# Performance work log

Measured on AMD Instinct MI355X. Metric: run time of the kernel, lower is better.

The kernel has to match this reference:

```python
import jax, jax.numpy as jnp
import numpy as np
from jax import lax

WINDOW_SIZE = 11
GAUSSIAN_SIGMA = 1.5
CROP_BORDER = 4
C1 = (0.01 * 255.0) ** 2
C2 = (0.03 * 255.0) ** 2


def _gaussian_kernel_window(ws: int, sigma: float) -> jnp.ndarray:
    # matches cv2.getGaussianKernel(ws, sigma) outer product
    x = jnp.arange(ws, dtype=jnp.float32) - (ws - 1) / 2.0
    g = jnp.exp(-(x ** 2) / (2.0 * sigma ** 2))
    g = g / jnp.sum(g)
    return jnp.outer(g, g)  # [ws, ws]


def _depthwise_conv(x: jnp.ndarray, kern: jnp.ndarray) -> jnp.ndarray:
    # x: [N, C, H, W]; kern: [C, 1, ws, ws]; valid padding, stride 1, groups=C
    return lax.conv_general_dilated(
        x, kern, window_strides=(1, 1), padding='VALID',
        dimension_numbers=('NCHW', 'OIHW', 'NCHW'),
        feature_group_count=x.shape[1])


def setup_inputs() -> dict:
    key = jax.random.key(0)
    k1, k2 = jax.random.split(key)
    raw_tensor = jax.random.uniform(k1, (32, 3, 512, 512), dtype=jnp.float32)
    dst_tensor = jax.random.uniform(k2, (32, 3, 512, 512), dtype=jnp.float32)
    return {"raw_tensor": raw_tensor, "dst_tensor": dst_tensor}


def reference(raw_tensor, dst_tensor):
    cb = CROP_BORDER
    raw = raw_tensor[:, :, cb:-cb, cb:-cb] * 255.0
    dst = dst_tensor[:, :, cb:-cb, cb:-cb] * 255.0
    C = raw.shape[1]
    kern = jnp.broadcast_to(
        _gaussian_kernel_window(WINDOW_SIZE, GAUSSIAN_SIGMA)[None, None],
        (C, 1, WINDOW_SIZE, WINDOW_SIZE)).astype(raw.dtype)

    raw_mean = _depthwise_conv(raw, kern)
    dst_mean = _depthwise_conv(dst, kern)
    raw_mean_sq = raw_mean ** 2
    dst_mean_sq = dst_mean ** 2
    raw_dst_mean = raw_mean * dst_mean
    raw_var = _depthwise_conv(raw * raw, kern) - raw_mean_sq
    dst_var = _depthwise_conv(dst * dst, kern) - dst_mean_sq
    raw_dst_cov = _depthwise_conv(raw * dst, kern) - raw_dst_mean

    num = (2.0 * raw_dst_mean + C1) * (2.0 * raw_dst_cov + C2)
    den = (raw_mean_sq + dst_mean_sq + C1) * (raw_var + dst_var + C2)
    ssim_map = num / den
    return jnp.mean(ssim_map, axis=(1, 2, 3)).astype(jnp.float32)  # [B]
```

## Files before the change

kernel.cpp:

```cpp
#include <hip/hip_runtime.h>


#define IMG   512
#define OUTD  494
#define CB    4
#define TW    64
#define TH    32
#define VSW   80
#define C1F   6.5025f
#define C2F   58.5225f
#define NPIX  732108.0f
#define XBLK  8
#define YBLK  16
#define SLOTS 384

__global__ __launch_bounds__(256) void ssim_main(
        const float* __restrict__ raw, const float* __restrict__ dst,
        float* __restrict__ partial) {
    __shared__ float vs[5][TH][VSW];
    __shared__ float red[4];

    const int tid = threadIdx.x;
    const int bc  = blockIdx.z;
    const int b   = bc / 3;
    const int c3  = bc - b * 3;
    const int ty0 = blockIdx.y * TH;
    const int tx0 = blockIdx.x * TW;

    float gw[11];
    {
        float s = 0.f;
        #pragma unroll
        for (int k = 0; k < 11; ++k) {
            float x = (float)(k - 5);
            gw[k] = expf(-x * x * (1.0f / 4.5f));
            s += gw[k];
        }
        float inv = 1.0f / s;
        #pragma unroll
        for (int k = 0; k < 11; ++k) gw[k] *= inv;
    }

    const float* rb = raw + (size_t)bc * (IMG * IMG);
    const float* db = dst + (size_t)bc * (IMG * IMG);

    #pragma unroll 1
    for (int t = tid; t < 304; t += 256) {
        const int rp = t / 19;
        const int xg = t - rp * 19;
        int col0 = CB + tx0 + xg * 4;
        if (col0 > IMG - 4) col0 = IMG - 4;
        const int row0 = CB + ty0 + rp * 2;

        float a0[5][4] = {{0.f}};
        float a1[5][4] = {{0.f}};
        #pragma unroll
        for (int k = 0; k < 12; ++k) {
            int r = row0 + k;
            if (r > IMG - 1) r = IMG - 1;
            const float4 va = *(const float4*)(rb + (size_t)r * IMG + col0);
            const float4 vc = *(const float4*)(db + (size_t)r * IMG + col0);
            const float A[4]  = {va.x, va.y, va.z, va.w};
            const float Cv[4] = {vc.x, vc.y, vc.z, vc.w};
            float p2[4], q2[4], pq[4];
            #pragma unroll
            for (int c = 0; c < 4; ++c) {
                p2[c] = A[c] * A[c];
                q2[c] = Cv[c] * Cv[c];
                pq[c] = A[c] * Cv[c];
            }
            if (k < 11) {
                const float w = gw[k];
                #pragma unroll
                for (int c = 0; c < 4; ++c) {
                    a0[0][c] = fmaf(w, A[c],  a0[0][c]);
                    a0[1][c] = fmaf(w, Cv[c], a0[1][c]);
                    a0[2][c] = fmaf(w, p2[c], a0[2][c]);
                    a0[3][c] = fmaf(w, q2[c], a0[3][c]);
                    a0[4][c] = fmaf(w, pq[c], a0[4][c]);
                }
            }
            if (k >= 1) {
                const float w = gw[k - 1];
                #pragma unroll
                for (int c = 0; c < 4; ++c) {
                    a1[0][c] = fmaf(w, A[c],  a1[0][c]);
                    a1[1][c] = fmaf(w, Cv[c], a1[1][c]);
                    a1[2][c] = fmaf(w, p2[c], a1[2][c]);
                    a1[3][c] = fmaf(w, q2[c], a1[3][c]);
                    a1[4][c] = fmaf(w, pq[c], a1[4][c]);
                }
            }
        }
        #pragma unroll
        for (int f = 0; f < 5; ++f) {
            *(float4*)&vs[f][rp * 2 + 0][xg * 4] =
                make_float4(a0[f][0], a0[f][1], a0[f][2], a0[f][3]);
            *(float4*)&vs[f][rp * 2 + 1][xg * 4] =
                make_float4(a1[f][0], a1[f][1], a1[f][2], a1[f][3]);
        }
    }
    __syncthreads();

    const int xg  = tid & 15;
    const int yt  = tid >> 4;
    const int ox0 = tx0 + xg * 4;
    float ssum = 0.f;
    #pragma unroll
    for (int r2 = 0; r2 < 2; ++r2) {
        const int row = yt * 2 + r2;
        const int oy  = ty0 + row;
        float m[5][4];
        #pragma unroll
        for (int f = 0; f < 5; ++f) {
            const float4* vp = (const float4*)&vs[f][row][xg * 4];
            const float4 A = vp[0], B = vp[1], Cq = vp[2], D = vp[3];
            const float win[16] = {A.x, A.y, A.z, A.w, B.x, B.y, B.z, B.w,
                                   Cq.x, Cq.y, Cq.z, Cq.w, D.x, D.y, D.z, D.w};
            #pragma unroll
            for (int c = 0; c < 4; ++c) {
                float o = 0.f;
                #pragma unroll
                for (int k = 0; k < 11; ++k) o = fmaf(gw[k], win[c + k], o);
                m[f][c] = o;
            }
        }
        if (oy < OUTD) {
            #pragma unroll
            for (int c = 0; c < 4; ++c) {
                if (ox0 + c < OUTD) {
                    const float mr  = m[0][c] * 255.0f;
                    const float md  = m[1][c] * 255.0f;
                    const float mrr = m[2][c] * 65025.0f;
                    const float mdd = m[3][c] * 65025.0f;
                    const float mrd = m[4][c] * 65025.0f;
                    const float mr2 = mr * mr, md2 = md * md, mpr = mr * md;
                    const float num = (2.0f * mpr + C1F) * (2.0f * (mrd - mpr) + C2F);
                    const float den = (mr2 + md2 + C1F) * ((mrr - mr2) + (mdd - md2) + C2F);
                    ssum += num / den;
                }
            }
        }
    }

    #pragma unroll
    for (int off = 32; off > 0; off >>= 1)
        ssum += __shfl_down(ssum, off, 64);
    const int lane = tid & 63, wv = tid >> 6;
    if (lane == 0) red[wv] = ssum;
    __syncthreads();
    if (tid == 0) {
        const float t = red[0] + red[1] + red[2] + red[3];
        partial[(size_t)b * SLOTS + (blockIdx.y * gridDim.x + blockIdx.x) * 3 + c3] = t;
    }
}

__global__ __launch_bounds__(128) void ssim_final(
        const float* __restrict__ partial, float* __restrict__ out) {
    __shared__ float red[2];
    const int b = blockIdx.x, tid = threadIdx.x;
    float s = 0.f;
    for (int i = tid; i < SLOTS; i += 128) s += partial[(size_t)b * SLOTS + i];
    #pragma unroll
    for (int off = 32; off > 0; off >>= 1) s += __shfl_down(s, off, 64);
    if ((tid & 63) == 0) red[tid >> 6] = s;
    __syncthreads();
    if (tid == 0) out[b] = (red[0] + red[1]) * (1.0f / NPIX);
}

extern "C" void kernel_launch(void* const* d_in, const int* in_sizes, int n_in,
                              void* d_out, int out_size, void* d_ws, size_t ws_size,
                              hipStream_t stream) {
    const float* raw = (const float*)d_in[0];
    const float* dst = (const float*)d_in[1];
    float* out     = (float*)d_out;
    float* partial = (float*)d_ws;

    dim3 grid(XBLK, YBLK, 96);
    ssim_main<<<grid, 256, 0, stream>>>(raw, dst, partial);
    ssim_final<<<32, 128, 0, stream>>>(partial, out);
}
```

Measured before the change: 275.1 us.

## Fold SSIM second-moment fields into sum-of-squares and squared-sum, widen horizontal pass

Replaces the three second-moment fields (r², d², rd) with two, r²+d² and (r+d)², so the covariance is recovered as ((r+d)² − (r²+d²))/2. This cuts the vertical-pass accumulators, the shared-memory intermediate and the horizontal convolutions from five fields to four. The horizontal pass now gives each thread one row of 8 outputs instead of two rows of 4, so neighbouring outputs share more of each loaded window. The launch bounds also request 4 blocks per SM, and the shared row stride shrinks. Recovering covariance by subtraction may cost some precision through cancellation.

```diff
diff --git a/kernel.cpp b/kernel.cpp
--- a/kernel.cpp
+++ b/kernel.cpp
@@ -6,7 +6,7 @@
 #define CB    4
 #define TW    64
 #define TH    32
-#define VSW   80
+#define VSW   76
 #define C1F   6.5025f
 #define C2F   58.5225f
 #define NPIX  732108.0f
@@ -14,10 +14,10 @@
 #define YBLK  16
 #define SLOTS 384
 
-__global__ __launch_bounds__(256) void ssim_main(
+__global__ __launch_bounds__(256, 4) void ssim_main(
         const float* __restrict__ raw, const float* __restrict__ dst,
         float* __restrict__ partial) {
-    __shared__ float vs[5][TH][VSW];
+    __shared__ float vs[4][TH][VSW];
     __shared__ float red[4];
 
     const int tid = threadIdx.x;
@@ -52,48 +52,46 @@
         if (col0 > IMG - 4) col0 = IMG - 4;
         const int row0 = CB + ty0 + rp * 2;
 
-        float a0[5][4] = {{0.f}};
-        float a1[5][4] = {{0.f}};
+        float a0[4][4] = {{0.f}};
+        float a1[4][4] = {{0.f}};
         #pragma unroll
         for (int k = 0; k < 12; ++k) {
             int r = row0 + k;
             if (r > IMG - 1) r = IMG - 1;
             const float4 va = *(const float4*)(rb + (size_t)r * IMG + col0);
             const float4 vc = *(const float4*)(db + (size_t)r * IMG + col0);
-            const float A[4]  = {va.x, va.y, va.z, va.w};
-            const float Cv[4] = {vc.x, vc.y, vc.z, vc.w};
-            float p2[4], q2[4], pq[4];
+            const float R[4] = {va.x, va.y, va.z, va.w};
+            const float D[4] = {vc.x, vc.y, vc.z, vc.w};
+            float s2[4], p2[4];
             #pragma unroll
             for (int c = 0; c < 4; ++c) {
-                p2[c] = A[c] * A[c];
-                q2[c] = Cv[c] * Cv[c];
-                pq[c] = A[c] * Cv[c];
+                const float u = R[c] + D[c];
+                s2[c] = fmaf(R[c], R[c], D[c] * D[c]);
+                p2[c] = u * u;
             }
             if (k < 11) {
                 const float w = gw[k];
                 #pragma unroll
                 for (int c = 0; c < 4; ++c) {
-                    a0[0][c] = fmaf(w, A[c],  a0[0][c]);
-                    a0[1][c] = fmaf(w, Cv[c], a0[1][c]);
-                    a0[2][c] = fmaf(w, p2[c], a0[2][c]);
-                    a0[3][c] = fmaf(w, q2[c], a0[3][c]);
-                    a0[4][c] = fmaf(w, pq[c], a0[4][c]);
+                    a0[0][c] = fmaf(w, R[c],  a0[0][c]);
+                    a0[1][c] = fmaf(w, D[c],  a0[1][c]);
+                    a0[2][c] = fmaf(w, s2[c], a0[2][c]);
+                    a0[3][c] = fmaf(w, p2[c], a0[3][c]);
                 }
             }
             if (k >= 1) {
                 const float w = gw[k - 1];
                 #pragma unroll
                 for (int c = 0; c < 4; ++c) {
-                    a1[0][c] = fmaf(w, A[c],  a1[0][c]);
-                    a1[1][c] = fmaf(w, Cv[c], a1[1][c]);
-                    a1[2][c] = fmaf(w, p2[c], a1[2][c]);
-                    a1[3][c] = fmaf(w, q2[c], a1[3][c]);
-                    a1[4][c] = fmaf(w, pq[c], a1[4][c]);
+                    a1[0][c] = fmaf(w, R[c],  a1[0][c]);
+                    a1[1][c] = fmaf(w, D[c],  a1[1][c]);
+                    a1[2][c] = fmaf(w, s2[c], a1[2][c]);
+                    a1[3][c] = fmaf(w, p2[c], a1[3][c]);
                 }
             }
         }
         #pragma unroll
-        for (int f = 0; f < 5; ++f) {
+        for (int f = 0; f < 4; ++f) {
             *(float4*)&vs[f][rp * 2 + 0][xg * 4] =
                 make_float4(a0[f][0], a0[f][1], a0[f][2], a0[f][3]);
             *(float4*)&vs[f][rp * 2 + 1][xg * 4] =
@@ -102,43 +100,43 @@
     }
     __syncthreads();
 
-    const int xg  = tid & 15;
-    const int yt  = tid >> 4;
-    const int ox0 = tx0 + xg * 4;
+    const int xg  = tid & 7;
+    const int row = tid >> 3;
+    const int ox0 = tx0 + xg * 8;
+    const int oy  = ty0 + row;
+
+    float m[4][8];
+    #pragma unroll
+    for (int f = 0; f < 4; ++f) {
+        const float4* vp = (const float4*)&vs[f][row][xg * 8];
+        const float4 A = vp[0], B = vp[1], Cq = vp[2], Dq = vp[3], Eq = vp[4];
+        const float win[20] = {A.x, A.y, A.z, A.w,  B.x, B.y, B.z, B.w,
+                               Cq.x, Cq.y, Cq.z, Cq.w, Dq.x, Dq.y, Dq.z, Dq.w,
+                               Eq.x, Eq.y, Eq.z, Eq.w};
+        #pragma unroll
+        for (int c = 0; c < 8; ++c) {
+            float o = 0.f;
+            #pragma unroll
+            for (int k = 0; k < 11; ++k) o = fmaf(gw[k], win[c + k], o);
+            m[f][c] = o;
+        }
+    }
+
     float ssum = 0.f;
-    #pragma unroll
-    for (int r2 = 0; r2 < 2; ++r2) {
-        const int row = yt * 2 + r2;
-        const int oy  = ty0 + row;
-        float m[5][4];
+    if (oy < OUTD) {
         #pragma unroll
-        for (int f = 0; f < 5; ++f) {
-            const float4* vp = (const float4*)&vs[f][row][xg * 4];
-            const float4 A = vp[0], B = vp[1], Cq = vp[2], D = vp[3];
-            const float win[16] = {A.x, A.y, A.z, A.w, B.x, B.y, B.z, B.w,
-                                   Cq.x, Cq.y, Cq.z, Cq.w, D.x, D.y, D.z, D.w};
-            #pragma unroll
-            for (int c = 0; c < 4; ++c) {
-                float o = 0.f;
-                #pragma unroll
-                for (int k = 0; k < 11; ++k) o = fmaf(gw[k], win[c + k], o);
-                m[f][c] = o;
-            }
-        }
-        if (oy < OUTD) {
-            #pragma unroll
-            for (int c = 0; c < 4; ++c) {
-                if (ox0 + c < OUTD) {
-                    const float mr  = m[0][c] * 255.0f;
-                    const float md  = m[1][c] * 255.0f;
-                    const float mrr = m[2][c] * 65025.0f;
-                    const float mdd = m[3][c] * 65025.0f;
-                    const float mrd = m[4][c] * 65025.0f;
-                    const float mr2 = mr * mr, md2 = md * md, mpr = mr * md;
-                    const float num = (2.0f * mpr + C1F) * (2.0f * (mrd - mpr) + C2F);
-                    const float den = (mr2 + md2 + C1F) * ((mrr - mr2) + (mdd - md2) + C2F);
-                    ssum += num / den;
-                }
+        for (int c = 0; c < 8; ++c) {
+            if (ox0 + c < OUTD) {
+                const float mr  = m[0][c] * 255.0f;
+                const float md  = m[1][c] * 255.0f;
+                const float S2  = m[2][c] * 65025.0f;
+                const float P2  = m[3][c] * 65025.0f;
+                const float mr2 = mr * mr, md2 = md * md, mpr = mr * md;
+                const float num = (2.0f * mpr + C1F) *
+                                  ((P2 - S2) - 2.0f * mpr + C2F);
+                const float den = (mr2 + md2 + C1F) *
+                                  ((S2 - mr2 - md2) + C2F);
+                ssum += num / den;
             }
         }
     }
```

Measured after the change: 266.5 us. -3.1%, faster.
